# Kernel optimization log

Hardware: AMD Instinct MI355X
Metric: run time of the kernel (lower is better)

Reference implementation:

```python
import jax, jax.numpy as jnp
import numpy as np

N = 100000      # nodes
E = 1600000     # edges (avg degree 16)
IN_C = 128
HID = 64
OUT_C = 2


def compute_norm(edge_index, n):
    """1/rowcount of M = I + A^T (distinct nonzeros per row, coalesce semantics)."""
    idt = edge_index.dtype
    ar = jnp.arange(n, dtype=idt)
    rows = jnp.concatenate([ar, edge_index[1]])  # M built from transposed edges
    cols = jnp.concatenate([ar, edge_index[0]])
    order = jnp.lexsort((cols, rows))
    rs, cs = rows[order], cols[order]
    uniq = jnp.concatenate([jnp.array([True]),
                            (rs[1:] != rs[:-1]) | (cs[1:] != cs[:-1])])
    rowcount = jnp.zeros((n,), jnp.float32).at[rs].add(uniq.astype(jnp.float32))
    return 1.0 / jnp.maximum(rowcount, 1.0)


def pan_conv(x, edge_index, w_lin, b_lin, w_pan, norm):
    # PyG PANConv, filter_size=1: out = diag(norm) @ (w0*I + w0*w1*A^T) @ (x W + b)
    h = x @ w_lin + b_lin                                   # [N, HID]
    src, dst = edge_index[0], edge_index[1]
    agg = jnp.zeros_like(h).at[dst].add(h[src])             # (A^T h)[i] = sum_{src->i} h[src]
    out = w_pan[0] * h + (w_pan[0] * w_pan[1]) * agg
    return norm[:, None] * out


def setup_inputs() -> dict:
    key = jax.random.key(0)
    ks = jax.random.split(key, 8)
    x = jax.random.normal(ks[0], (N, IN_C), jnp.float32)
    edge_index = jax.random.randint(ks[1], (2, E), 0, N, dtype=jnp.int32)
    w1_lin = jax.random.normal(ks[2], (IN_C, HID), jnp.float32) * 0.05
    b1_lin = jnp.zeros((HID,), jnp.float32)
    w1_pan = jax.random.uniform(ks[3], (2,), jnp.float32, 0.5, 1.5)
    w2_lin = jax.random.normal(ks[4], (HID, HID), jnp.float32) * 0.05
    b2_lin = jnp.zeros((HID,), jnp.float32)
    w2_pan = jax.random.uniform(ks[5], (2,), jnp.float32, 0.5, 1.5)
    wc = jax.random.normal(ks[6], (2 * HID, OUT_C), jnp.float32) * 0.05
    bc = jnp.zeros((OUT_C,), jnp.float32)
    return {"x": x, "edge_index": edge_index,
            "w1_lin": w1_lin, "b1_lin": b1_lin, "w1_pan": w1_pan,
            "w2_lin": w2_lin, "b2_lin": b2_lin, "w2_pan": w2_pan,
            "wc": wc, "bc": bc}


def reference(x, edge_index, w1_lin, b1_lin, w1_pan, w2_lin, b2_lin, w2_pan, wc, bc):
    n = x.shape[0]
    norm = compute_norm(edge_index, n)          # graph-structure only; shared by both layers
    h = pan_conv(x, edge_index, w1_lin, b1_lin, w1_pan, norm)
    h = jax.nn.relu(h)
    h = pan_conv(h, edge_index, w2_lin, b2_lin, w2_pan, norm)
    row, col = edge_index[0], edge_index[1]
    emb = jnp.concatenate([h[row], h[col]], axis=-1)  # [E, 2*HID]
    return emb @ wc + bc                               # [E, OUT_C]
```

## Files before the change

kernel.cpp:

```cpp
#include <hip/hip_runtime.h>
#include <hip/hip_bf16.h>

#define NNODES 100000
#define NEDGES 1600000
#define INC 128
#define HIDC 64
#define BSHIFT 7
#define NB ((NNODES + 127) / 128)
#define TILE 4096
#define HSLOTS 4096
#define CAP 4096
#define CAPE 4096
#define NBLK_FILL ((NEDGES + TILE - 1) / TILE)
#define NBLK_LIN ((NNODES + 63) / 64)

typedef short bf16x8 __attribute__((ext_vector_type(8)));
typedef float f32x4 __attribute__((ext_vector_type(4)));

__device__ __forceinline__ float bf2f(unsigned short h) {
    return __uint_as_float((unsigned)h << 16);
}
__device__ __forceinline__ unsigned short f2bf(float f) {
    __hip_bfloat16 h = __float2bfloat16(f);
    return *(unsigned short*)&h;
}

__global__ __launch_bounds__(256) void prep_w_kernel(
        const float* __restrict__ w1, unsigned short* __restrict__ wTh,
        unsigned short* __restrict__ wTl,
        const float* __restrict__ w2_lin, const float* __restrict__ b2,
        const float* __restrict__ wc, float* __restrict__ w44,
        float* __restrict__ bias4, unsigned short* __restrict__ out) {
    int t = threadIdx.x;
    int e = blockIdx.x * 256 + t;
    int c = e >> 7, k = e & 127;
    float v = w1[k * 64 + c];
    unsigned short hi = f2bf(v);
    wTh[e] = hi;
    wTl[e] = f2bf(v - bf2f(hi));
    if (blockIdx.x == 0) {
        if (t < 16)
            *(ushort4*)(out + (size_t)NNODES * 64 + t * 4) = make_ushort4(0, 0, 0, 0);
        int kk = t >> 2, j = t & 3;
        float a = 0.0f;
#pragma unroll 8
        for (int i = 0; i < 64; i++) {
            float w4 = (j < 2) ? wc[i * 2 + j] : wc[(64 + i) * 2 + (j - 2)];
            a += w2_lin[kk * 64 + i] * w4;
        }
        w44[kk * 4 + j] = a;
        if (kk == 0) {
            float bb4 = 0.0f;
            for (int i = 0; i < 64; i++) {
                float w4 = (j < 2) ? wc[i * 2 + j] : wc[(64 + i) * 2 + (j - 2)];
                bb4 += b2[i] * w4;
            }
            bias4[j] = bb4;
        }
    }
}

__global__ __launch_bounds__(256, 5) void fat_kernel(
        const float* __restrict__ x,
        const unsigned short* __restrict__ wTh, const unsigned short* __restrict__ wTl,
        const float* __restrict__ b, unsigned short* __restrict__ out,
        const int* __restrict__ src, const int* __restrict__ dst,
        int* __restrict__ bucket_fill, unsigned int* __restrict__ staging) {
    __shared__ alignas(16) unsigned char smem[32768];
    int t = threadIdx.x;
    if (blockIdx.x < NBLK_FILL) {
        int* cnt = (int*)smem;
        int* basepos = cnt + NB;
        unsigned int* svl = (unsigned int*)(basepos + NB);
        for (int i = t; i < NB; i += 256) cnt[i] = 0;
        int tile0 = blockIdx.x * TILE;
        int se[16], de[16];
#pragma unroll
        for (int i = 0; i < 16; i++) {
            int e = tile0 + i * 256 + t;
            if (e < NEDGES) { se[i] = src[e]; de[i] = dst[e]; }
            else            { se[i] = -1;     de[i] = 0; }
        }
        __syncthreads();
        int meta[16];
#pragma unroll
        for (int i = 0; i < 16; i++) {
            meta[i] = -1;
            if (se[i] >= 0) {
                int bkt = de[i] >> BSHIFT;
                int r = atomicAdd(&cnt[bkt], 1);
                meta[i] = (bkt << 12) | r;
                svl[i * 256 + t] = ((unsigned)(de[i] & 127) << 17) | (unsigned)se[i];
            }
        }
        __syncthreads();
        for (int i = t; i < NB; i += 256) {
            int c = cnt[i];
            int g = (c > 0) ? atomicAdd(&bucket_fill[i], c) : 0;
            basepos[i] = (i << 12) + g;
        }
        __syncthreads();
#pragma unroll
        for (int i = 0; i < 16; i++) {
            if (meta[i] >= 0) {
                int bkt = meta[i] >> 12, r = meta[i] & 4095;
                staging[basepos[bkt] + r] = svl[i * 256 + t];
            }
        }
    } else {
        unsigned short* s_bh = (unsigned short*)smem;
        unsigned short* s_bl = s_bh + 64 * 128;
        int node0 = (blockIdx.x - NBLK_FILL) * 64;
        int l = t & 63, wv = t >> 6;
        int mr = l & 15, g = l >> 4;
        int arow = wv * 16 + mr;
        int node = node0 + arow;
        bool vr = (node < NNODES);
        const float* xr = x + (size_t)node * INC;
        float4 vx[8];
#pragma unroll
        for (int ks = 0; ks < 4; ks++) {
            int k0 = ks * 32 + g * 8;
            vx[2 * ks]     = vr ? *(const float4*)(xr + k0)
                                : make_float4(0.f, 0.f, 0.f, 0.f);
            vx[2 * ks + 1] = vr ? *(const float4*)(xr + k0 + 4)
                                : make_float4(0.f, 0.f, 0.f, 0.f);
        }
#pragma unroll
        for (int i = 0; i < 4; i++) {
            int e = i * 256 + t;
            uint4 vh = *(const uint4*)(wTh + (size_t)e * 8);
            uint4 vl = *(const uint4*)(wTl + (size_t)e * 8);
            int col = e >> 4, k0 = (e & 15) * 8;
            int ke = k0 ^ ((col & 7) << 3);
            *(uint4*)&s_bh[col * 128 + ke] = vh;
            *(uint4*)&s_bl[col * 128 + ke] = vl;
        }
        __syncthreads();
        f32x4 acc[4] = {{0.f, 0.f, 0.f, 0.f}, {0.f, 0.f, 0.f, 0.f},
                        {0.f, 0.f, 0.f, 0.f}, {0.f, 0.f, 0.f, 0.f}};
#pragma unroll
        for (int ks = 0; ks < 4; ks++) {
            int k0 = ks * 32 + g * 8;
            float xv[8] = {vx[2 * ks].x, vx[2 * ks].y, vx[2 * ks].z, vx[2 * ks].w,
                           vx[2 * ks + 1].x, vx[2 * ks + 1].y,
                           vx[2 * ks + 1].z, vx[2 * ks + 1].w};
            bf16x8 ah, al;
#pragma unroll
            for (int j = 0; j < 8; j++) {
                unsigned short h = f2bf(xv[j]);
                ah[j] = (short)h;
                al[j] = (short)f2bf(xv[j] - bf2f(h));
            }
#pragma unroll
            for (int cb = 0; cb < 4; cb++) {
                int col = cb * 16 + mr;
                int ko = k0 ^ ((col & 7) << 3);
                bf16x8 bh = *(const bf16x8*)&s_bh[col * 128 + ko];
                bf16x8 bl = *(const bf16x8*)&s_bl[col * 128 + ko];
                acc[cb] = __builtin_amdgcn_mfma_f32_16x16x32_bf16(ah, bh, acc[cb], 0, 0, 0);
                acc[cb] = __builtin_amdgcn_mfma_f32_16x16x32_bf16(ah, bl, acc[cb], 0, 0, 0);
                acc[cb] = __builtin_amdgcn_mfma_f32_16x16x32_bf16(al, bh, acc[cb], 0, 0, 0);
            }
        }
#pragma unroll
        for (int cb = 0; cb < 4; cb++) {
            int col = cb * 16 + mr;
            float bb = b[col];
#pragma unroll
            for (int r = 0; r < 4; r++) {
                int n2 = node0 + wv * 16 + g * 4 + r;
                if (n2 < NNODES)
                    out[(size_t)n2 * 64 + col] = f2bf(acc[cb][r] + bb);
            }
        }
    }
}

__global__ __launch_bounds__(256) void fill2_kernel(
        const int* __restrict__ bucket_fill, const unsigned int* __restrict__ staging,
        int* __restrict__ csr_src, int* __restrict__ row_start,
        int* __restrict__ row_pdeg, float* __restrict__ norm, int n_nodes) {
    __shared__ int cnt[128];
    __shared__ int dcount[128];
    __shared__ int off[128];
    __shared__ int pscan[128];
    __shared__ unsigned short rank16[CAP];
    __shared__ unsigned int ht[HSLOTS];
    int t = threadIdx.x;
    int b = blockIdx.x;
    int node0 = b << BSHIFT;
    int nn = min(128, n_nodes - node0);
    if (t < 128) { cnt[t] = 0; dcount[t] = 0; }
    {
        uint4* h4 = (uint4*)ht;
        uint4 ff = make_uint4(0xFFFFFFFFu, 0xFFFFFFFFu, 0xFFFFFFFFu, 0xFFFFFFFFu);
        for (int i = t; i < HSLOTS / 4; i += 256) h4[i] = ff;
    }
    __syncthreads();
    int start = b << 12;
    int total = bucket_fill[b];
    for (int li = t; li < total; li += 256) {
        unsigned int w = staging[start + li];
        int s = (int)(w & 0x1FFFFu);
        int dl = (int)(w >> 17);
        int r = atomicAdd(&cnt[dl], 1);
        rank16[li] = (unsigned short)r;
        if (s != node0 + dl) {
            unsigned int slot = ((w * 2654435761u) >> 13) & (HSLOTS - 1);
            while (true) {
                unsigned int prev = atomicCAS(&ht[slot], 0xFFFFFFFFu, w);
                if (prev == 0xFFFFFFFFu) { atomicAdd(&dcount[dl], 1); break; }
                if (prev == w) break;
                slot = (slot + 1) & (HSLOTS - 1);
            }
        }
    }
    __syncthreads();
    int cv = 0, pv = 0;
    if (t < 128) {
        cv = cnt[t];
        pv = (cv + 7) & ~7;
        pscan[t] = pv;
    }
    __syncthreads();
    for (int o = 1; o < 128; o <<= 1) {
        int xx = (t >= o && t < 128) ? pscan[t - o] : 0;
        __syncthreads();
        if (t < 128) pscan[t] += xx;
        __syncthreads();
    }
    if (t < 128) off[t] = b * CAPE + pscan[t] - pv;
    __syncthreads();
    if (t < nn) {
        row_start[node0 + t] = off[t];
        row_pdeg[node0 + t] = pv;
        norm[node0 + t] = 1.0f / (1.0f + (float)dcount[t]);
    }
    if (t < 128)
        for (int k = cv; k < pv; k++) csr_src[off[t] + k] = n_nodes << 7;
    for (int li = t; li < total; li += 256) {
        unsigned int w = staging[start + li];
        int s = (int)(w & 0x1FFFFu);
        int dl = (int)(w >> 17);
        csr_src[off[dl] + (int)rank16[li]] = s << 7;
    }
}

__global__ void agg_h_kernel(const unsigned int* __restrict__ lin32,
                             const int* __restrict__ row_start,
                             const int* __restrict__ row_pdeg,
                             const int* __restrict__ csr_src,
                             const float* __restrict__ norm,
                             const float* __restrict__ wpan, const float* __restrict__ w44,
                             const float* __restrict__ bias4, float* __restrict__ u,
                             int n_nodes) {
    int t = threadIdx.x;
    int lane = t & 63;
    int sl = lane & 31;
    int h5 = lane >> 5;
    int quad = blockIdx.x * 4 + (t >> 6);
    if (blockIdx.x == 0 && t < 4) u[n_nodes * 4 + t] = 0.0f;
    int nX = quad * 4 + h5 * 2;
    int nY = nX + 1;
    int e0X = row_start[nX], pdX = row_pdeg[nX];
    int e0Y = row_start[nY], pdY = row_pdeg[nY];
    int pm = max(pdX, pdY);
    int pmax = max(pm, __shfl_xor(pm, 32));
    int sentB = n_nodes << 7;
    unsigned sl4 = (unsigned)sl * 4;
    const char* base8 = (const char*)lin32;
    float xL0 = 0.f, xH0 = 0.f, xL1 = 0.f, xH1 = 0.f;
    float yL0 = 0.f, yH0 = 0.f, yL1 = 0.f, yH1 = 0.f;
    for (int base = 0; base < pmax; base += 32) {
        int li = base + sl;
        int soX = (li < pdX) ? csr_src[e0X + li] : sentB;
        int soY = (li < pdY) ? csr_src[e0Y + li] : sentB;
        int m = min(32, pmax - base);
#pragma unroll
        for (int i = 0; i < 32; i += 2) {
            if (i < m) {
                int xA0 = __builtin_amdgcn_readlane(soX, i);
                int xB0 = __builtin_amdgcn_readlane(soX, 32 + i);
                int xA1 = __builtin_amdgcn_readlane(soX, i + 1);
                int xB1 = __builtin_amdgcn_readlane(soX, 33 + i);
                int yA0 = __builtin_amdgcn_readlane(soY, i);
                int yB0 = __builtin_amdgcn_readlane(soY, 32 + i);
                int yA1 = __builtin_amdgcn_readlane(soY, i + 1);
                int yB1 = __builtin_amdgcn_readlane(soY, 33 + i);
                int ox0 = h5 ? xB0 : xA0;
                int ox1 = h5 ? xB1 : xA1;
                int oy0 = h5 ? yB0 : yA0;
                int oy1 = h5 ? yB1 : yA1;
                unsigned int wx0 = *(const unsigned int*)(base8 + (unsigned)(ox0 + sl4));
                unsigned int wx1 = *(const unsigned int*)(base8 + (unsigned)(ox1 + sl4));
                unsigned int wy0 = *(const unsigned int*)(base8 + (unsigned)(oy0 + sl4));
                unsigned int wy1 = *(const unsigned int*)(base8 + (unsigned)(oy1 + sl4));
                xL0 += __uint_as_float(wx0 << 16);
                xH0 += __uint_as_float(wx0 & 0xFFFF0000u);
                xL1 += __uint_as_float(wx1 << 16);
                xH1 += __uint_as_float(wx1 & 0xFFFF0000u);
                yL0 += __uint_as_float(wy0 << 16);
                yH0 += __uint_as_float(wy0 & 0xFFFF0000u);
                yL1 += __uint_as_float(wy1 << 16);
                yH1 += __uint_as_float(wy1 & 0xFFFF0000u);
            }
        }
    }
    float aLX = xL0 + xL1, aHX = xH0 + xH1;
    float aLY = yL0 + yL1, aHY = yH0 + yH1;
    unsigned int wsX = *(const unsigned int*)(base8 + (unsigned)((nX << 7) + sl4));
    unsigned int wsY = *(const unsigned int*)(base8 + (unsigned)((nY << 7) + sl4));
    float nrX = norm[nX], nrY = norm[nY];
    float w0 = wpan[0];
    float w01 = wpan[0] * wpan[1];
    float vLX = fmaxf(nrX * (w0 * __uint_as_float(wsX << 16) + w01 * aLX), 0.0f);
    float vHX = fmaxf(nrX * (w0 * __uint_as_float(wsX & 0xFFFF0000u) + w01 * aHX), 0.0f);
    float vLY = fmaxf(nrY * (w0 * __uint_as_float(wsY << 16) + w01 * aLY), 0.0f);
    float vHY = fmaxf(nrY * (w0 * __uint_as_float(wsY & 0xFFFF0000u) + w01 * aHY), 0.0f);
    int c0 = 2 * sl;
    float4 wv0 = *(const float4*)(w44 + c0 * 4);
    float4 wv1 = *(const float4*)(w44 + (c0 + 1) * 4);
    float pX0 = vLX * wv0.x + vHX * wv1.x;
    float pX1 = vLX * wv0.y + vHX * wv1.y;
    float pX2 = vLX * wv0.z + vHX * wv1.z;
    float pX3 = vLX * wv0.w + vHX * wv1.w;
    float pY0 = vLY * wv0.x + vHY * wv1.x;
    float pY1 = vLY * wv0.y + vHY * wv1.y;
    float pY2 = vLY * wv0.z + vHY * wv1.z;
    float pY3 = vLY * wv0.w + vHY * wv1.w;
    for (int off = 16; off; off >>= 1) {
        pX0 += __shfl_xor(pX0, off);
        pX1 += __shfl_xor(pX1, off);
        pX2 += __shfl_xor(pX2, off);
        pX3 += __shfl_xor(pX3, off);
        pY0 += __shfl_xor(pY0, off);
        pY1 += __shfl_xor(pY1, off);
        pY2 += __shfl_xor(pY2, off);
        pY3 += __shfl_xor(pY3, off);
    }
    if (sl == 0) {
        float4 bb = *(const float4*)bias4;
        *(float4*)(u + nX * 4) =
            make_float4(pX0 + bb.x, pX1 + bb.y, pX2 + bb.z, pX3 + bb.w);
    }
    if (sl == 1) {
        float4 bb = *(const float4*)bias4;
        *(float4*)(u + nY * 4) =
            make_float4(pY0 + bb.x, pY1 + bb.y, pY2 + bb.z, pY3 + bb.w);
    }
}

__global__ void agg_pq4_kernel(const float* __restrict__ u, const int* __restrict__ row_start,
                               const int* __restrict__ row_pdeg,
                               const int* __restrict__ csr_src,
                               const float* __restrict__ norm,
                               const float* __restrict__ wpan, float* __restrict__ pq,
                               int n_nodes) {
    int t = threadIdx.x;
    int node = blockIdx.x * 64 + (t >> 2);
    int j = t & 3;
    if (node >= n_nodes) return;
    int e0 = row_start[node];
    int pd = row_pdeg[node];
    float acc = 0.0f;
    for (int e = 0; e < pd; e += 8) {
#pragma unroll
        for (int k = 0; k < 8; k++) {
            int so = csr_src[e0 + e + k];
            acc += u[(so >> 5) + j];
        }
    }
    float w0 = wpan[0];
    float w01 = wpan[0] * wpan[1];
    pq[node * 4 + j] = norm[node] * (w0 * u[node * 4 + j] + w01 * acc);
}

__global__ void edge_out_kernel(const int* __restrict__ src, const int* __restrict__ dst,
                                const float* __restrict__ pq, const float* __restrict__ bc,
                                float* __restrict__ out, int n_edges) {
    int e = blockIdx.x * blockDim.x + threadIdx.x;
    if (e >= n_edges) return;
    int r = src[e], c = dst[e];
    float2 p = *(const float2*)(pq + r * 4);
    float2 q = *(const float2*)(pq + c * 4 + 2);
    float2 o = make_float2(p.x + q.x + bc[0], p.y + q.y + bc[1]);
    *(float2*)(out + e * 2) = o;
}

extern "C" void kernel_launch(void* const* d_in, const int* in_sizes, int n_in,
                              void* d_out, int out_size, void* d_ws, size_t ws_size,
                              hipStream_t stream) {
    const float* x      = (const float*)d_in[0];
    const int*   eidx   = (const int*)d_in[1];
    const float* w1_lin = (const float*)d_in[2];
    const float* b1_lin = (const float*)d_in[3];
    const float* w1_pan = (const float*)d_in[4];
    const float* w2_lin = (const float*)d_in[5];
    const float* b2_lin = (const float*)d_in[6];
    const float* w2_pan = (const float*)d_in[7];
    const float* wc     = (const float*)d_in[8];
    const float* bc     = (const float*)d_in[9];
    float* out = (float*)d_out;

    const int* src = eidx;
    const int* dst = eidx + NEDGES;

    char* ws = (char*)d_ws;
    size_t off = 0;
    auto carve = [&](size_t bytes) {
        char* p = ws + off;
        off = (off + bytes + 255) & ~(size_t)255;
        return p;
    };
    int*   bucket_fill = (int*)carve((size_t)NB * 4);
    int*   row_start = (int*)carve((size_t)NNODES * 4);
    int*   row_pdeg  = (int*)carve((size_t)NNODES * 4);
    unsigned int* staging = (unsigned int*)carve((size_t)NB * CAP * 4);
    int*   csr_src  = (int*)carve(((size_t)NB * CAPE + 256) * 4);
    float* nrm      = (float*)carve((size_t)NNODES * 4);
    unsigned short* bufA = (unsigned short*)carve((size_t)(NNODES + 1) * HIDC * 2);
    float* u        = (float*)carve((size_t)(NNODES + 1) * 4 * 4);
    float* pq       = (float*)carve((size_t)NNODES * 4 * 4);
    float* w44      = (float*)carve((size_t)64 * 4 * 4);
    float* bias4    = (float*)carve((size_t)4 * 4);
    unsigned short* wTh = (unsigned short*)carve((size_t)HIDC * INC * 2);
    unsigned short* wTl = (unsigned short*)carve((size_t)HIDC * INC * 2);
    (void)ws_size; (void)in_sizes; (void)n_in; (void)out_size;

    hipMemsetAsync(bucket_fill, 0, (size_t)NB * 4, stream);

    prep_w_kernel<<<32, 256, 0, stream>>>(w1_lin, wTh, wTl, w2_lin, b2_lin, wc,
                                          w44, bias4, bufA);

    fat_kernel<<<NBLK_FILL + NBLK_LIN, 256, 0, stream>>>(
        x, wTh, wTl, b1_lin, bufA, src, dst, bucket_fill, staging);

    fill2_kernel<<<NB, 256, 0, stream>>>(bucket_fill, staging, csr_src, row_start, row_pdeg,
                                         nrm, NNODES);

    agg_h_kernel<<<(NNODES / 16), 256, 0, stream>>>(
        (const unsigned int*)bufA, row_start, row_pdeg, csr_src, nrm, w1_pan, w44, bias4,
        u, NNODES);

    agg_pq4_kernel<<<(NNODES + 63) / 64, 256, 0, stream>>>(
        u, row_start, row_pdeg, csr_src, nrm, w2_pan, pq, NNODES);

    edge_out_kernel<<<NEDGES / 256, 256, 0, stream>>>(src, dst, pq, bc, out, NEDGES);
}
```

Baseline: 226.5 us.

## Regroup prep, CSR fill and GEMM kernels into two fused launches

Weight preparation is merged with the edge-bucketing pass (fill1) into one launch. The node linear GEMM is merged with the CSR build pass (fill2) into a second launch. This cuts one kernel launch and lets the independent GEMM run alongside CSR construction. In exchange, the fill2 blocks now share the GEMM's 32KB shared-memory footprint and its launch bounds, which may change occupancy.

```diff
diff --git a/kernel.cpp b/kernel.cpp
--- a/kernel.cpp
+++ b/kernel.cpp
@@ -13,6 +13,7 @@
 #define CAPE 4096
 #define NBLK_FILL ((NEDGES + TILE - 1) / TILE)
 #define NBLK_LIN ((NNODES + 63) / 64)
+#define NPREP 32
 
 typedef short bf16x8 __attribute__((ext_vector_type(8)));
 typedef float f32x4 __attribute__((ext_vector_type(4)));
@@ -25,55 +26,49 @@
     return *(unsigned short*)&h;
 }
 
-__global__ __launch_bounds__(256) void prep_w_kernel(
+__global__ __launch_bounds__(256) void prepfill1_kernel(
         const float* __restrict__ w1, unsigned short* __restrict__ wTh,
         unsigned short* __restrict__ wTl,
         const float* __restrict__ w2_lin, const float* __restrict__ b2,
         const float* __restrict__ wc, float* __restrict__ w44,
-        float* __restrict__ bias4, unsigned short* __restrict__ out) {
+        float* __restrict__ bias4, unsigned short* __restrict__ out,
+        const int* __restrict__ src, const int* __restrict__ dst,
+        int* __restrict__ bucket_fill, unsigned int* __restrict__ staging) {
+    __shared__ alignas(16) unsigned char smem[22528];
     int t = threadIdx.x;
-    int e = blockIdx.x * 256 + t;
-    int c = e >> 7, k = e & 127;
-    float v = w1[k * 64 + c];
-    unsigned short hi = f2bf(v);
-    wTh[e] = hi;
-    wTl[e] = f2bf(v - bf2f(hi));
-    if (blockIdx.x == 0) {
-        if (t < 16)
-            *(ushort4*)(out + (size_t)NNODES * 64 + t * 4) = make_ushort4(0, 0, 0, 0);
-        int kk = t >> 2, j = t & 3;
-        float a = 0.0f;
+    if (blockIdx.x < NPREP) {
+        int e = blockIdx.x * 256 + t;
+        int c = e >> 7, k = e & 127;
+        float v = w1[k * 64 + c];
+        unsigned short hi = f2bf(v);
+        wTh[e] = hi;
+        wTl[e] = f2bf(v - bf2f(hi));
+        if (blockIdx.x == 0) {
+            if (t < 16)
+                *(ushort4*)(out + (size_t)NNODES * 64 + t * 4) = make_ushort4(0, 0, 0, 0);
+            int kk = t >> 2, j = t & 3;
+            float a = 0.0f;
 #pragma unroll 8
-        for (int i = 0; i < 64; i++) {
-            float w4 = (j < 2) ? wc[i * 2 + j] : wc[(64 + i) * 2 + (j - 2)];
-            a += w2_lin[kk * 64 + i] * w4;
-        }
-        w44[kk * 4 + j] = a;
-        if (kk == 0) {
-            float bb4 = 0.0f;
             for (int i = 0; i < 64; i++) {
                 float w4 = (j < 2) ? wc[i * 2 + j] : wc[(64 + i) * 2 + (j - 2)];
-                bb4 += b2[i] * w4;
-            }
-            bias4[j] = bb4;
-        }
-    }
-}
-
-__global__ __launch_bounds__(256, 5) void fat_kernel(
-        const float* __restrict__ x,
-        const unsigned short* __restrict__ wTh, const unsigned short* __restrict__ wTl,
-        const float* __restrict__ b, unsigned short* __restrict__ out,
-        const int* __restrict__ src, const int* __restrict__ dst,
-        int* __restrict__ bucket_fill, unsigned int* __restrict__ staging) {
-    __shared__ alignas(16) unsigned char smem[32768];
-    int t = threadIdx.x;
-    if (blockIdx.x < NBLK_FILL) {
+                a += w2_lin[kk * 64 + i] * w4;
+            }
+            w44[kk * 4 + j] = a;
+            if (kk == 0) {
+                float bb4 = 0.0f;
+                for (int i = 0; i < 64; i++) {
+                    float w4 = (j < 2) ? wc[i * 2 + j] : wc[(64 + i) * 2 + (j - 2)];
+                    bb4 += b2[i] * w4;
+                }
+                bias4[j] = bb4;
+            }
+        }
+    } else {
         int* cnt = (int*)smem;
         int* basepos = cnt + NB;
         unsigned int* svl = (unsigned int*)(basepos + NB);
         for (int i = t; i < NB; i += 256) cnt[i] = 0;
-        int tile0 = blockIdx.x * TILE;
+        int tile0 = (blockIdx.x - NPREP) * TILE;
         int se[16], de[16];
 #pragma unroll
         for (int i = 0; i < 16; i++) {
@@ -107,10 +102,22 @@
                 staging[basepos[bkt] + r] = svl[i * 256 + t];
             }
         }
-    } else {
+    }
+}
+
+__global__ __launch_bounds__(256, 5) void gemmfill2_kernel(
+        const float* __restrict__ x,
+        const unsigned short* __restrict__ wTh, const unsigned short* __restrict__ wTl,
+        const float* __restrict__ b, unsigned short* __restrict__ out,
+        const int* __restrict__ bucket_fill, const unsigned int* __restrict__ staging,
+        int* __restrict__ csr_src, int* __restrict__ row_start,
+        int* __restrict__ row_pdeg, float* __restrict__ norm, int n_nodes) {
+    __shared__ alignas(16) unsigned char smem[32768];
+    int t = threadIdx.x;
+    if (blockIdx.x < NBLK_LIN) {
         unsigned short* s_bh = (unsigned short*)smem;
         unsigned short* s_bl = s_bh + 64 * 128;
-        int node0 = (blockIdx.x - NBLK_FILL) * 64;
+        int node0 = blockIdx.x * 64;
         int l = t & 63, wv = t >> 6;
         int mr = l & 15, g = l >> 4;
         int arow = wv * 16 + mr;
@@ -174,76 +181,70 @@
                     out[(size_t)n2 * 64 + col] = f2bf(acc[cb][r] + bb);
             }
         }
-    }
-}
-
-__global__ __launch_bounds__(256) void fill2_kernel(
-        const int* __restrict__ bucket_fill, const unsigned int* __restrict__ staging,
-        int* __restrict__ csr_src, int* __restrict__ row_start,
-        int* __restrict__ row_pdeg, float* __restrict__ norm, int n_nodes) {
-    __shared__ int cnt[128];
-    __shared__ int dcount[128];
-    __shared__ int off[128];
-    __shared__ int pscan[128];
-    __shared__ unsigned short rank16[CAP];
-    __shared__ unsigned int ht[HSLOTS];
-    int t = threadIdx.x;
-    int b = blockIdx.x;
-    int node0 = b << BSHIFT;
-    int nn = min(128, n_nodes - node0);
-    if (t < 128) { cnt[t] = 0; dcount[t] = 0; }
-    {
-        uint4* h4 = (uint4*)ht;
-        uint4 ff = make_uint4(0xFFFFFFFFu, 0xFFFFFFFFu, 0xFFFFFFFFu, 0xFFFFFFFFu);
-        for (int i = t; i < HSLOTS / 4; i += 256) h4[i] = ff;
-    }
-    __syncthreads();
-    int start = b << 12;
-    int total = bucket_fill[b];
-    for (int li = t; li < total; li += 256) {
-        unsigned int w = staging[start + li];
-        int s = (int)(w & 0x1FFFFu);
-        int dl = (int)(w >> 17);
-        int r = atomicAdd(&cnt[dl], 1);
-        rank16[li] = (unsigned short)r;
-        if (s != node0 + dl) {
-            unsigned int slot = ((w * 2654435761u) >> 13) & (HSLOTS - 1);
-            while (true) {
-                unsigned int prev = atomicCAS(&ht[slot], 0xFFFFFFFFu, w);
-                if (prev == 0xFFFFFFFFu) { atomicAdd(&dcount[dl], 1); break; }
-                if (prev == w) break;
-                slot = (slot + 1) & (HSLOTS - 1);
-            }
-        }
-    }
-    __syncthreads();
-    int cv = 0, pv = 0;
-    if (t < 128) {
-        cv = cnt[t];
-        pv = (cv + 7) & ~7;
-        pscan[t] = pv;
-    }
-    __syncthreads();
-    for (int o = 1; o < 128; o <<= 1) {
-        int xx = (t >= o && t < 128) ? pscan[t - o] : 0;
-        __syncthreads();
-        if (t < 128) pscan[t] += xx;
-        __syncthreads();
-    }
-    if (t < 128) off[t] = b * CAPE + pscan[t] - pv;
-    __syncthreads();
-    if (t < nn) {
-        row_start[node0 + t] = off[t];
-        row_pdeg[node0 + t] = pv;
-        norm[node0 + t] = 1.0f / (1.0f + (float)dcount[t]);
-    }
-    if (t < 128)
-        for (int k = cv; k < pv; k++) csr_src[off[t] + k] = n_nodes << 7;
-    for (int li = t; li < total; li += 256) {
-        unsigned int w = staging[start + li];
-        int s = (int)(w & 0x1FFFFu);
-        int dl = (int)(w >> 17);
-        csr_src[off[dl] + (int)rank16[li]] = s << 7;
+    } else {
+        int* cnt = (int*)smem;
+        int* dcount = cnt + 128;
+        int* off = dcount + 128;
+        int* pscan = off + 128;
+        unsigned short* rank16 = (unsigned short*)(pscan + 128);
+        unsigned int* ht = (unsigned int*)(rank16 + CAP);
+        int b2k = blockIdx.x - NBLK_LIN;
+        int node0 = b2k << BSHIFT;
+        int nn = min(128, n_nodes - node0);
+        if (t < 128) { cnt[t] = 0; dcount[t] = 0; }
+        {
+            uint4* h4 = (uint4*)ht;
+            uint4 ff = make_uint4(0xFFFFFFFFu, 0xFFFFFFFFu, 0xFFFFFFFFu, 0xFFFFFFFFu);
+            for (int i = t; i < HSLOTS / 4; i += 256) h4[i] = ff;
+        }
+        __syncthreads();
+        int start = b2k << 12;
+        int total = bucket_fill[b2k];
+        for (int li = t; li < total; li += 256) {
+            unsigned int w = staging[start + li];
+            int s = (int)(w & 0x1FFFFu);
+            int dl = (int)(w >> 17);
+            int r = atomicAdd(&cnt[dl], 1);
+            rank16[li] = (unsigned short)r;
+            if (s != node0 + dl) {
+                unsigned int slot = ((w * 2654435761u) >> 13) & (HSLOTS - 1);
+                while (true) {
+                    unsigned int prev = atomicCAS(&ht[slot], 0xFFFFFFFFu, w);
+                    if (prev == 0xFFFFFFFFu) { atomicAdd(&dcount[dl], 1); break; }
+                    if (prev == w) break;
+                    slot = (slot + 1) & (HSLOTS - 1);
+                }
+            }
+        }
+        __syncthreads();
+        int cv = 0, pv = 0;
+        if (t < 128) {
+            cv = cnt[t];
+            pv = (cv + 7) & ~7;
+            pscan[t] = pv;
+        }
+        __syncthreads();
+        for (int o = 1; o < 128; o <<= 1) {
+            int xx = (t >= o && t < 128) ? pscan[t - o] : 0;
+            __syncthreads();
+            if (t < 128) pscan[t] += xx;
+            __syncthreads();
+        }
+        if (t < 128) off[t] = b2k * CAPE + pscan[t] - pv;
+        __syncthreads();
+        if (t < nn) {
+            row_start[node0 + t] = off[t];
+            row_pdeg[node0 + t] = pv;
+            norm[node0 + t] = 1.0f / (1.0f + (float)dcount[t]);
+        }
+        if (t < 128)
+            for (int k = cv; k < pv; k++) csr_src[off[t] + k] = n_nodes << 7;
+        for (int li = t; li < total; li += 256) {
+            unsigned int w = staging[start + li];
+            int s = (int)(w & 0x1FFFFu);
+            int dl = (int)(w >> 17);
+            csr_src[off[dl] + (int)rank16[li]] = s << 7;
+        }
     }
 }
 
@@ -430,14 +431,13 @@
 
     hipMemsetAsync(bucket_fill, 0, (size_t)NB * 4, stream);
 
-    prep_w_kernel<<<32, 256, 0, stream>>>(w1_lin, wTh, wTl, w2_lin, b2_lin, wc,
-                                          w44, bias4, bufA);
-
-    fat_kernel<<<NBLK_FILL + NBLK_LIN, 256, 0, stream>>>(
-        x, wTh, wTl, b1_lin, bufA, src, dst, bucket_fill, staging);
-
-    fill2_kernel<<<NB, 256, 0, stream>>>(bucket_fill, staging, csr_src, row_start, row_pdeg,
-                                         nrm, NNODES);
+    prepfill1_kernel<<<NPREP + NBLK_FILL, 256, 0, stream>>>(
+        w1_lin, wTh, wTl, w2_lin, b2_lin, wc, w44, bias4, bufA,
+        src, dst, bucket_fill, staging);
+
+    gemmfill2_kernel<<<NBLK_LIN + NB, 256, 0, stream>>>(
+        x, wTh, wTl, b1_lin, bufA,
+        bucket_fill, staging, csr_src, row_start, row_pdeg, nrm, NNODES);
 
     agg_h_kernel<<<(NNODES / 16), 256, 0, stream>>>(
         (const unsigned int*)bufA, row_start, row_pdeg, csr_src, nrm, w1_pan, w44, bias4,
```

Result: no change. 222.4 us (-1.8%).
